# Performance work log

Measured on AMD Instinct MI355X. Metric: run time of the kernel, lower is better.

Reference implementation:

```python
import jax, jax.numpy as jnp
import numpy as np

V, E, H2, T = 50000, 256, 512, 16  # vocab, embed, hidden_dim, tagset
H = H2 // 2                        # per-direction hidden
START, STOP = 14, 15
NEG = -10000.0


def setup_inputs() -> dict:
    key = jax.random.key(0)
    ks = jax.random.split(key, 13)
    s = 0.08
    tokens = jax.random.randint(ks[0], (32, 512), 0, V)
    embed_table = jax.random.normal(ks[1], (V, E), jnp.float32)
    Wi_f = jax.random.normal(ks[2], (4 * H, E), jnp.float32) * s
    Wh_f = jax.random.normal(ks[3], (4 * H, H), jnp.float32) * s
    bi_f = jnp.zeros((4 * H,), jnp.float32)
    bh_f = jnp.zeros((4 * H,), jnp.float32)
    Wi_b = jax.random.normal(ks[4], (4 * H, E), jnp.float32) * s
    Wh_b = jax.random.normal(ks[5], (4 * H, H), jnp.float32) * s
    bi_b = jnp.zeros((4 * H,), jnp.float32)
    bh_b = jnp.zeros((4 * H,), jnp.float32)
    Wt = jax.random.normal(ks[6], (T, H2), jnp.float32) * s
    bt = jnp.zeros((T,), jnp.float32)
    trans = jax.random.normal(ks[7], (T, T), jnp.float32)
    trans = trans.at[START, :].set(NEG).at[:, STOP].set(NEG)
    return {"tokens": tokens, "embed_table": embed_table,
            "Wi_f": Wi_f, "Wh_f": Wh_f, "bi_f": bi_f, "bh_f": bh_f,
            "Wi_b": Wi_b, "Wh_b": Wh_b, "bi_b": bi_b, "bh_b": bh_b,
            "Wt": Wt, "bt": bt, "transitions": trans}


def _lstm_dir(x, Wi, Wh, bi, bh, reverse=False):
    # x: [S, B, E] -> h seq [S, B, H], PyTorch gate order i,f,g,o
    S, B, _ = x.shape
    xs = x[::-1] if reverse else x
    pre = jnp.einsum('sbe,ge->sbg', xs, Wi) + bi + bh  # precompute input GEMM

    def step(carry, z_t):
        h, c = carry
        z = z_t + h @ Wh.T  # [B, 4H]
        i, f, g, o = jnp.split(z, 4, axis=-1)
        c = jax.nn.sigmoid(f) * c + jax.nn.sigmoid(i) * jnp.tanh(g)
        h = jax.nn.sigmoid(o) * jnp.tanh(c)
        return (h, c), h

    h0 = jnp.zeros((B, H), x.dtype)
    _, hs = jax.lax.scan(step, (h0, h0), pre)
    return hs[::-1] if reverse else hs


def reference(tokens, embed_table, Wi_f, Wh_f, bi_f, bh_f,
              Wi_b, Wh_b, bi_b, bh_b, Wt, bt, transitions):
    x = embed_table[tokens]                # [B, S, E]
    x = jnp.transpose(x, (1, 0, 2))        # [S, B, E] seq-first like nn.LSTM
    hf = _lstm_dir(x, Wi_f, Wh_f, bi_f, bh_f, reverse=False)
    hb = _lstm_dir(x, Wi_b, Wh_b, bi_b, bh_b, reverse=True)
    feats = jnp.concatenate([hf, hb], axis=-1)           # [S, B, 2H]
    emissions = jnp.einsum('sbh,th->sbt', feats, Wt) + bt  # [S, B, T]

    B = tokens.shape[0]
    alpha0 = jnp.full((B, T), NEG, jnp.float32).at[:, START].set(0.0)

    def crf_step(alpha, emit_t):
        # alpha: [B, T_prev]; transitions[next, prev]; emit_t: [B, T_next]
        scores = alpha[:, None, :] + transitions[None, :, :] + emit_t[:, :, None]
        return jax.nn.logsumexp(scores, axis=2), None

    alpha, _ = jax.lax.scan(crf_step, alpha0, emissions)
    log_Z = jax.nn.logsumexp(alpha + transitions[STOP][None, :], axis=1)  # [B]
    return log_Z
```

## Files before the change

### kernel.cpp

```cpp
#include <hip/hip_runtime.h>
#include <hip/hip_bf16.h>
#include <stdint.h>

typedef __attribute__((ext_vector_type(4))) float f32x4;
typedef __attribute__((ext_vector_type(8))) short bf16x8;

#define SENT 0xFFFFFFFFFFFFFFFFULL

#define WS_XBF   0u
#define WS_WIR   8388608u
#define WS_BIAS  9437184u
#define WS_PRE   9445376u
#define WS_HALL  76554240u
#define WS_CTL   93364224u
#define WS_EMIS  93368320u
#define WS_CHK   94416896u
#define WS_FLG   WS_CHK

__device__ __forceinline__ unsigned short f2bf(float x) {
    union { float f; unsigned int u; } v; v.f = x;
    return (unsigned short)((v.u + 0x7FFFu + ((v.u >> 16) & 1u)) >> 16);
}
__device__ __forceinline__ float bf2f(unsigned short b) {
    union { float f; unsigned int u; } v; v.u = ((unsigned int)b) << 16; return v.f;
}
__device__ __forceinline__ unsigned int pack2(float a, float b) {
    return (unsigned int)f2bf(a) | ((unsigned int)f2bf(b) << 16);
}
__device__ __forceinline__ float sigf(float x)  { return 1.0f / (1.0f + __expf(-x)); }
__device__ __forceinline__ float tanhf_(float x){ return 1.0f - 2.0f / (__expf(2.0f * x) + 1.0f); }

__global__ __launch_bounds__(256) void k_prep(
    const int* __restrict__ tokens, const float* __restrict__ embed,
    const float* __restrict__ Wi_f, const float* __restrict__ Wi_b,
    const float* __restrict__ bi_f, const float* __restrict__ bh_f,
    const float* __restrict__ bi_b, const float* __restrict__ bh_b,
    char* __restrict__ ws)
{
    int blk = blockIdx.x, tid = threadIdx.x;
    unsigned short* xbf  = (unsigned short*)(ws + WS_XBF);
    unsigned short* wir  = (unsigned short*)(ws + WS_WIR);
    float* biasr         = (float*)(ws + WS_BIAS);
    if (blk < 2048) {
        int rr = tid >> 5, cc = tid & 31;
        int r = blk * 8 + rr;
        int s = r >> 5, b = r & 31;
        int tok = tokens[b * 512 + s];
        int k = cc * 8;
        const float* src = embed + (size_t)tok * 256 + k;
        float4 a = *(const float4*)src;
        float4 c = *(const float4*)(src + 4);
        uint4 o; o.x = pack2(a.x, a.y); o.y = pack2(a.z, a.w);
        o.z = pack2(c.x, c.y); o.w = pack2(c.z, c.w);
        *(uint4*)(xbf + (size_t)r * 256 + k) = o;
    } else if (blk < 2304) {
        int rr = tid >> 5, cc = tid & 31;
        int rowp = (blk - 2048) * 8 + rr;
        int dir = rowp >> 10, q = rowp & 1023;
        int j = q >> 8, rs = q & 255;
        int g = rs >> 6, hl = rs & 63;
        int srow = g * 256 + j * 64 + hl;
        const float* W = dir ? Wi_b : Wi_f;
        int k = cc * 8;
        const float* src = W + (size_t)srow * 256 + k;
        float4 a = *(const float4*)src;
        float4 c = *(const float4*)(src + 4);
        uint4 o; o.x = pack2(a.x, a.y); o.y = pack2(a.z, a.w);
        o.z = pack2(c.x, c.y); o.w = pack2(c.z, c.w);
        *(uint4*)(wir + (size_t)rowp * 256 + k) = o;
        if (cc == 0)
            biasr[rowp] = dir ? (bi_b[srow] + bh_b[srow]) : (bi_f[srow] + bh_f[srow]);
    } else {
        if (blk == 2304 && tid < 16)
            ((unsigned int*)(ws + WS_CTL))[tid] = 0u;
        if (blk == 2305) {
            unsigned int* flg = (unsigned int*)(ws + WS_FLG);
            for (int u = tid; u < 2 * 513 * 4 * 16; u += 256) flg[u] = 0u;
        }
        size_t g = (size_t)(blk - 2304) * 256 + tid;
        uint4* hall4 = (uint4*)(ws + WS_HALL);
        const unsigned int NF = 0xFFFFFFFFu;
        for (size_t u = g; u < 1050624u; u += 65536u) {
            size_t slot = (u >> 10) % 513u;
            uint4 val;
            if (slot == 0) { val.x = 0u; val.y = 0u; val.z = 0u; val.w = 0u; }
            else           { val.x = NF; val.y = NF; val.z = NF; val.w = NF; }
            hall4[u] = val;
        }
    }
}

__global__ __launch_bounds__(256) void k_pregemm(char* __restrict__ ws)
{
    __shared__ unsigned short Asb[128 * 136];
    __shared__ unsigned short Bsb[64 * 136];
    const unsigned short* xbf = (const unsigned short*)(ws + WS_XBF);
    const unsigned short* wir = (const unsigned short*)(ws + WS_WIR);
    const float* biasr        = (const float*)(ws + WS_BIAS);
    unsigned short* pre       = (unsigned short*)(ws + WS_PRE);
    int blk = blockIdx.x, tid = threadIdx.x;
    int mb = blk >> 5, nb = blk & 31;
    int Mbase = mb * 128, Nbase = nb * 64;
    int w = tid >> 6, l = tid & 63, col = l & 15, quad = l >> 4;
    f32x4 acc[4][2];
    #pragma unroll
    for (int a = 0; a < 4; ++a)
        #pragma unroll
        for (int b = 0; b < 2; ++b) acc[a][b] = (f32x4){0.f, 0.f, 0.f, 0.f};

    for (int kh = 0; kh < 2; ++kh) {
        __syncthreads();
        #pragma unroll
        for (int i = 0; i < 8; ++i) {
            int c = tid + i * 256;
            int row = c >> 4, c16 = c & 15;
            uint4 v = *(const uint4*)(xbf + ((size_t)(Mbase + row) * 256 + kh * 128 + c16 * 8));
            *(uint4*)(Asb + row * 136 + c16 * 8) = v;
        }
        #pragma unroll
        for (int i = 0; i < 4; ++i) {
            int c = tid + i * 256;
            int row = c >> 4, c16 = c & 15;
            uint4 v = *(const uint4*)(wir + ((size_t)(Nbase + row) * 256 + kh * 128 + c16 * 8));
            *(uint4*)(Bsb + row * 136 + c16 * 8) = v;
        }
        __syncthreads();
        int mhalf = w >> 1, nh = w & 1;
        #pragma unroll
        for (int kt = 0; kt < 4; ++kt) {
            bf16x8 bfr[2];
            #pragma unroll
            for (int nn = 0; nn < 2; ++nn)
                bfr[nn] = *(const bf16x8*)(Bsb + (16 * (nh * 2 + nn) + col) * 136 + kt * 32 + quad * 8);
            #pragma unroll
            for (int mm = 0; mm < 4; ++mm) {
                bf16x8 afr = *(const bf16x8*)(Asb + (16 * (mhalf * 4 + mm) + col) * 136 + kt * 32 + quad * 8);
                #pragma unroll
                for (int nn = 0; nn < 2; ++nn)
                    acc[mm][nn] = __builtin_amdgcn_mfma_f32_16x16x32_bf16(afr, bfr[nn], acc[mm][nn], 0, 0, 0);
            }
        }
    }
    #pragma unroll
    for (int mm = 0; mm < 4; ++mm) {
        int m_t = (w >> 1) * 4 + mm;
        int s = (Mbase >> 5) + (m_t >> 1);
        int bhalf = m_t & 1;
        #pragma unroll
        for (int nn = 0; nn < 2; ++nn) {
            int ncol = Nbase + 16 * ((w & 1) * 2 + nn) + col;
            int dir = ncol >> 10, j = (ncol >> 8) & 3, r = ncol & 255;
            int g = r >> 6, hl16 = (r >> 4) & 3;
            int tidp = (bhalf * 4 + hl16) * 64 + l;
            float bv = biasr[ncol];
            f32x4 a = acc[mm][nn];
            uint2 o;
            o.x = pack2(a[0] + bv, a[1] + bv);
            o.y = pack2(a[2] + bv, a[3] + bv);
            size_t off = (((size_t)(dir * 512 + s) * 4 + j) * 512 + tidp) * 16 + g * 4;
            *(uint2*)(pre + off) = o;
        }
    }
}

__global__ __launch_bounds__(512, 2) void k_rec(
    const float* __restrict__ Wh_f, const float* __restrict__ Wh_b, char* __restrict__ ws)
{
    __shared__ unsigned short hbuf[32 * 264];
    __shared__ unsigned short hst[8 * 16 * 20];
    __shared__ int sRole;
    int tid = threadIdx.x;

    if (tid == 0) {
        int xcd;
        asm volatile("s_getreg_b32 %0, hwreg(HW_REG_XCC_ID)" : "=s"(xcd));
        xcd &= 7;
        unsigned int* ctl = (unsigned int*)(ws + WS_CTL);
        unsigned int slot = __hip_atomic_fetch_add(&ctl[xcd], 1u,
                              __ATOMIC_RELAXED, __HIP_MEMORY_SCOPE_AGENT);
        int role = -1;
        if (slot < 8u) {
            if (slot == 7u) {
                unsigned int expv = 0u;
                __hip_atomic_compare_exchange_strong(&ctl[8], &expv, (unsigned int)(xcd + 1),
                    __ATOMIC_RELAXED, __ATOMIC_RELAXED, __HIP_MEMORY_SCOPE_AGENT);
            }
            unsigned int ts; long gc = 0;
            do {
                ts = __hip_atomic_fetch_add(&ctl[8], 0u,
                        __ATOMIC_RELAXED, __HIP_MEMORY_SCOPE_AGENT);
            } while (ts == 0u && ++gc < (1L << 26));
            if (ts == (unsigned int)(xcd + 1)) role = (int)slot;
        }
        sRole = role;
    }
    __syncthreads();
    int role = sRole;
    if (role < 0) return;
    int dir = role >> 2, j = role & 3;

    int w = tid >> 6, l = tid & 63, col = l & 15, quad = l >> 4;
    int m = w >> 2, hl16 = w & 3;
    const float* Wh = dir ? Wh_b : Wh_f;
    const unsigned short* pre = (const unsigned short*)(ws + WS_PRE);
    unsigned short* hall      = (unsigned short*)(ws + WS_HALL);
    unsigned int* flags       = (unsigned int*)(ws + WS_FLG);

    bf16x8 wf[4][8];
    #pragma unroll
    for (int g = 0; g < 4; ++g) {
        int grow = g * 256 + j * 64 + hl16 * 16 + col;
        #pragma unroll
        for (int kt = 0; kt < 8; ++kt) {
            const float* src = Wh + (size_t)grow * 256 + kt * 32 + quad * 8;
            float4 x0 = *(const float4*)src;
            float4 x1 = *(const float4*)(src + 4);
            bf16x8 f;
            f[0] = (short)f2bf(x0.x); f[1] = (short)f2bf(x0.y);
            f[2] = (short)f2bf(x0.z); f[3] = (short)f2bf(x0.w);
            f[4] = (short)f2bf(x1.x); f[5] = (short)f2bf(x1.y);
            f[6] = (short)f2bf(x1.z); f[7] = (short)f2bf(x1.w);
            wf[g][kt] = f;
        }
    }
    for (int u = tid; u < 1280; u += 512) ((unsigned int*)hst)[u] = 0;
    __syncthreads();

    float cst[4] = {0.f, 0.f, 0.f, 0.f};
    size_t hbase_u = (size_t)dir * 513 * 8192;
    int row0 = tid >> 6, c8 = tid & 63;
    bool ownl = (c8 >= j * 16) && (c8 < j * 16 + 16);
    int pollj = (l < 4 && l != j) ? l : -1;

    for (int st = 0; st < 512; ++st) {
        int s = dir ? (511 - st) : st;
        const uint4* pp = (const uint4*)(pre + ((((size_t)(dir * 512 + s)) * 4 + j) * 512 + tid) * 16);
        uint4 p0 = pp[0], p1 = pp[1];

        unsigned short* hsl = hall + hbase_u + (size_t)st * 8192;

        if (st > 0) {
            unsigned int* fl = flags + ((size_t)(dir * 513 + st)) * 64;
            int got = (pollj < 0) ? 1 : 0;
            int rnd = 0;
            while (!__all(got)) {
                if (!got) {
                    unsigned int expv = 0u;
                    __hip_atomic_compare_exchange_strong(fl + pollj * 16, &expv, 0u,
                        __ATOMIC_RELAXED, __ATOMIC_RELAXED, __HIP_MEMORY_SCOPE_WORKGROUP);
                    got = (expv != 0u) ? 1 : 0;
                }
                if (++rnd > (1 << 20)) break;
            }
            asm volatile("" ::: "memory");
        }

        unsigned long long v[4];
        if (ownl) {
            int lc = c8 * 4 - j * 64;
            int hl = lc >> 4, c4 = lc & 15;
            #pragma unroll
            for (int i = 0; i < 4; ++i) {
                int row = row0 + i * 8;
                int wp = (row >> 4) * 4 + hl, r_in = row & 15;
                v[i] = *(const unsigned long long*)(hst + wp * 320 + r_in * 20 + c4);
            }
        } else {
            #pragma unroll
            for (int i = 0; i < 4; ++i)
                v[i] = *(const unsigned long long*)(hsl + (size_t)(tid + i * 512) * 4);
        }
        #pragma unroll
        for (int i = 0; i < 4; ++i)
            *(unsigned long long*)(hbuf + (row0 + i * 8) * 264 + c8 * 4) = v[i];
        __syncthreads();

        f32x4 acc[4];
        #pragma unroll
        for (int g = 0; g < 4; ++g) acc[g] = (f32x4){0.f, 0.f, 0.f, 0.f};
        #pragma unroll
        for (int kt = 0; kt < 8; ++kt) {
            bf16x8 af = *(const bf16x8*)(hbuf + (m * 16 + col) * 264 + kt * 32 + quad * 8);
            #pragma unroll
            for (int g = 0; g < 4; ++g)
                acc[g] = __builtin_amdgcn_mfma_f32_16x16x32_bf16(af, wf[g][kt], acc[g], 0, 0, 0);
        }
        unsigned int pw[8] = {p0.x, p0.y, p0.z, p0.w, p1.x, p1.y, p1.z, p1.w};
        float z[4][4];
        #pragma unroll
        for (int g = 0; g < 4; ++g) {
            #pragma unroll
            for (int r2 = 0; r2 < 2; ++r2) {
                unsigned int u = pw[g * 2 + r2];
                z[g][r2 * 2]     = acc[g][r2 * 2]     + bf2f((unsigned short)(u & 0xffff));
                z[g][r2 * 2 + 1] = acc[g][r2 * 2 + 1] + bf2f((unsigned short)(u >> 16));
            }
        }
        unsigned short hb16[4];
        #pragma unroll
        for (int r = 0; r < 4; ++r) {
            float ci = sigf(z[1][r]) * cst[r] + sigf(z[0][r]) * tanhf_(z[2][r]);
            cst[r] = ci;
            hb16[r] = f2bf(sigf(z[3][r]) * tanhf_(ci));
        }
        unsigned short* hw = hst + w * 320;
        #pragma unroll
        for (int r = 0; r < 4; ++r) hw[(quad * 4 + r) * 20 + col] = hb16[r];
        int rrow = l >> 2, cpart = l & 3;
        unsigned long long hv = *(const unsigned long long*)(hw + rrow * 20 + cpart * 4);
        size_t dsto = hbase_u + (size_t)(st + 1) * 8192 + (size_t)(m * 16 + rrow) * 256
                    + j * 64 + hl16 * 16 + cpart * 4;
        *(unsigned long long*)(hall + dsto) = hv;
        __syncthreads();
        if (tid == 0)
            (void)__hip_atomic_exchange(flags + ((size_t)(dir * 513 + st + 1)) * 64 + j * 16, 1u,
                                        __ATOMIC_RELAXED, __HIP_MEMORY_SCOPE_WORKGROUP);
    }
}

__global__ __launch_bounds__(256) void k_emis(
    const float* __restrict__ Wt, const float* __restrict__ bt, char* __restrict__ ws)
{
    __shared__ float WtL[16 * 528];
    __shared__ unsigned short hrow[16 * 536];
    __shared__ float btL[16];
    int blk = blockIdx.x, tid = threadIdx.x;
    int sbb = blk * 16;
    int s = sbb >> 5, bbase = sbb & 31;
    const unsigned short* hall = (const unsigned short*)(ws + WS_HALL);
    float* emis = (float*)(ws + WS_EMIS);
    #pragma unroll
    for (int i = 0; i < 8; ++i) {
        int c = tid + i * 256;
        int trow = c >> 7, c128 = c & 127;
        float4 v = *(const float4*)(Wt + (size_t)trow * 512 + c128 * 4);
        *(float4*)(WtL + trow * 528 + c128 * 4) = v;
    }
    #pragma unroll
    for (int i = 0; i < 4; ++i) {
        int c = tid + i * 256;
        int row = c >> 6, c6 = c & 63, half = c6 >> 5, c16 = c6 & 31;
        size_t base = half == 0 ? (size_t)(s + 1) * 8192 : ((size_t)513 + (512 - s)) * 8192;
        uint4 v = *(const uint4*)(hall + base + (size_t)(bbase + row) * 256 + c16 * 8);
        *(uint4*)(hrow + row * 536 + half * 256 + c16 * 8) = v;
    }
    if (tid < 16) btL[tid] = bt[tid];
    __syncthreads();
    int t = tid >> 4, i = tid & 15;
    float acc = btL[t];
    const float* wrow = WtL + t * 528;
    const unsigned short* hr = hrow + i * 536;
    #pragma unroll 8
    for (int k = 0; k < 512; k += 4) {
        uint2 hu = *(const uint2*)(hr + k);
        float4 wv = *(const float4*)(wrow + k);
        acc += bf2f((unsigned short)(hu.x & 0xffff)) * wv.x
             + bf2f((unsigned short)(hu.x >> 16))    * wv.y
             + bf2f((unsigned short)(hu.y & 0xffff)) * wv.z
             + bf2f((unsigned short)(hu.y >> 16))    * wv.w;
    }
    emis[((size_t)(bbase + i) * 512 + s) * 16 + t] = acc;
}

__global__ __launch_bounds__(256) void k_crfc(const float* __restrict__ trans, char* __restrict__ ws)
{
    __shared__ float trL[16 * 17];
    __shared__ float est[16 * 16];
    __shared__ float Pb[2][16 * 17];
    int blk = blockIdx.x, tid = threadIdx.x;
    int b = blk >> 5, c = blk & 31;
    int t = tid >> 4, p = tid & 15;
    const float* emis = (const float*)(ws + WS_EMIS);
    float* chk = (float*)(ws + WS_CHK);
    trL[t * 17 + p] = trans[t * 16 + p];
    est[t * 16 + p] = emis[((size_t)b * 512 + c * 16 + t) * 16 + p];
    __syncthreads();
    float tr[16];
    #pragma unroll
    for (int q = 0; q < 16; ++q) tr[q] = trL[t * 17 + q];
    float out = trL[t * 17 + p] + est[0 * 16 + t];
    Pb[0][t * 17 + p] = out;
    __syncthreads();
    int cur = 0;
    for (int si = 1; si < 16; ++si) {
        float v[16]; float mx = -3.0e38f;
        #pragma unroll
        for (int q = 0; q < 16; ++q) { v[q] = tr[q] + Pb[cur][q * 17 + p]; mx = fmaxf(mx, v[q]); }
        float ss = 0.f;
        #pragma unroll
        for (int q = 0; q < 16; ++q) ss += __expf(v[q] - mx);
        out = est[si * 16 + t] + mx + __logf(ss);
        Pb[1 - cur][t * 17 + p] = out;
        __syncthreads();
        cur = 1 - cur;
    }
    chk[(size_t)(b * 32 + c) * 256 + t * 16 + p] = out;
}

__global__ __launch_bounds__(256) void k_crff(
    const float* __restrict__ trans, char* __restrict__ ws, float* __restrict__ out)
{
    __shared__ float Cst[16 * 17];
    __shared__ float Pb[2][16 * 17];
    __shared__ float af[16];
    int b = blockIdx.x, tid = threadIdx.x;
    int t = tid >> 4, p = tid & 15;
    const float* chk = (const float*)(ws + WS_CHK);
    Pb[0][t * 17 + p] = chk[(size_t)(b * 32) * 256 + t * 16 + p];
    __syncthreads();
    int cur = 0;
    for (int ci = 1; ci < 32; ++ci) {
        Cst[t * 17 + p] = chk[(size_t)(b * 32 + ci) * 256 + t * 16 + p];
        __syncthreads();
        float v[16]; float mx = -3.0e38f;
        #pragma unroll
        for (int q = 0; q < 16; ++q) { v[q] = Cst[t * 17 + q] + Pb[cur][q * 17 + p]; mx = fmaxf(mx, v[q]); }
        float ss = 0.f;
        #pragma unroll
        for (int q = 0; q < 16; ++q) ss += __expf(v[q] - mx);
        float outv = mx + __logf(ss);
        Pb[1 - cur][t * 17 + p] = outv;
        __syncthreads();
        cur = 1 - cur;
    }
    float vfin = Pb[cur][t * 17 + p] + ((p == 14) ? 0.0f : -10000.0f);
    Cst[t * 17 + p] = vfin;
    __syncthreads();
    if (tid < 16) {
        float mx = -3.0e38f;
        for (int q = 0; q < 16; ++q) mx = fmaxf(mx, Cst[tid * 17 + q]);
        float ss = 0.f;
        for (int q = 0; q < 16; ++q) ss += __expf(Cst[tid * 17 + q] - mx);
        af[tid] = mx + __logf(ss) + trans[15 * 16 + tid];
    }
    __syncthreads();
    if (tid == 0) {
        float mx = -3.0e38f;
        for (int q = 0; q < 16; ++q) mx = fmaxf(mx, af[q]);
        float ss = 0.f;
        for (int q = 0; q < 16; ++q) ss += __expf(af[q] - mx);
        out[b] = mx + __logf(ss);
    }
}

extern "C" void kernel_launch(void* const* d_in, const int* in_sizes, int n_in,
                              void* d_out, int out_size, void* d_ws, size_t ws_size,
                              hipStream_t stream)
{
    const int*   tokens = (const int*)d_in[0];
    const float* embed  = (const float*)d_in[1];
    const float* Wi_f   = (const float*)d_in[2];
    const float* Wh_f   = (const float*)d_in[3];
    const float* bi_f   = (const float*)d_in[4];
    const float* bh_f   = (const float*)d_in[5];
    const float* Wi_b   = (const float*)d_in[6];
    const float* Wh_b   = (const float*)d_in[7];
    const float* bi_b   = (const float*)d_in[8];
    const float* bh_b   = (const float*)d_in[9];
    const float* Wt     = (const float*)d_in[10];
    const float* bt     = (const float*)d_in[11];
    const float* trans  = (const float*)d_in[12];
    char* ws = (char*)d_ws;
    float* out = (float*)d_out;

    hipLaunchKernelGGL(k_prep, dim3(2560), dim3(256), 0, stream,
                       tokens, embed, Wi_f, Wi_b, bi_f, bh_f, bi_b, bh_b, ws);
    hipLaunchKernelGGL(k_pregemm, dim3(4096), dim3(256), 0, stream, ws);
    hipLaunchKernelGGL(k_rec, dim3(128), dim3(512), 0, stream, Wh_f, Wh_b, ws);
    hipLaunchKernelGGL(k_emis, dim3(1024), dim3(256), 0, stream, Wt, bt, ws);
    hipLaunchKernelGGL(k_crfc, dim3(1024), dim3(256), 0, stream, trans, ws);
    hipLaunchKernelGGL(k_crff, dim3(32), dim3(256), 0, stream, trans, ws, out);
}
```

Baseline: 1.814 ms.

## Read recurrent hidden state directly from global memory, pad LDS to force one block per CU

The recurrent LSTM kernel stops staging h through the LDS hbuf/hst buffers and loads the MFMA A-fragments straight from the global hidden-state history. Each lane now writes its bf16 h values with scalar stores, and the pre-step syncthreads and own-slice LDS path are removed. A large static and dynamic LDS padding is added so only one workgroup fits per CU, presumably to spread the cross-block spinning recurrence across more CUs. The spin-wait bound is lowered and the sentinel init is set to zero. The risks are scattered 2-byte global stores, and global reads that may see another block's rows before they are visible, since only relaxed flags guard them.

After: 2.198 ms. 1.21x slower.

```diff
diff --git a/kernel.cpp b/kernel.cpp
--- a/kernel.cpp
+++ b/kernel.cpp
@@ -4,8 +4,6 @@
 
 typedef __attribute__((ext_vector_type(4))) float f32x4;
 typedef __attribute__((ext_vector_type(8))) short bf16x8;
-
-#define SENT 0xFFFFFFFFFFFFFFFFULL
 
 #define WS_XBF   0u
 #define WS_WIR   8388608u
@@ -79,12 +77,11 @@
         }
         size_t g = (size_t)(blk - 2304) * 256 + tid;
         uint4* hall4 = (uint4*)(ws + WS_HALL);
-        const unsigned int NF = 0xFFFFFFFFu;
         for (size_t u = g; u < 1050624u; u += 65536u) {
             size_t slot = (u >> 10) % 513u;
             uint4 val;
             if (slot == 0) { val.x = 0u; val.y = 0u; val.z = 0u; val.w = 0u; }
-            else           { val.x = NF; val.y = NF; val.z = NF; val.w = NF; }
+            else           { val.x = 0u; val.y = 0u; val.z = 0u; val.w = 0u; }
             hall4[u] = val;
         }
     }
@@ -166,12 +163,14 @@
 __global__ __launch_bounds__(512, 2) void k_rec(
     const float* __restrict__ Wh_f, const float* __restrict__ Wh_b, char* __restrict__ ws)
 {
-    __shared__ unsigned short hbuf[32 * 264];
-    __shared__ unsigned short hst[8 * 16 * 20];
+    extern __shared__ char dynpad[];
+    __shared__ char stpad[61440];
     __shared__ int sRole;
     int tid = threadIdx.x;
 
     if (tid == 0) {
+        ((volatile char*)stpad)[0] = 0;
+        ((volatile char*)dynpad)[0] = 0;
         int xcd;
         asm volatile("s_getreg_b32 %0, hwreg(HW_REG_XCC_ID)" : "=s"(xcd));
         xcd &= 7;
@@ -223,21 +222,15 @@
             wf[g][kt] = f;
         }
     }
-    for (int u = tid; u < 1280; u += 512) ((unsigned int*)hst)[u] = 0;
-    __syncthreads();
 
     float cst[4] = {0.f, 0.f, 0.f, 0.f};
     size_t hbase_u = (size_t)dir * 513 * 8192;
-    int row0 = tid >> 6, c8 = tid & 63;
-    bool ownl = (c8 >= j * 16) && (c8 < j * 16 + 16);
     int pollj = (l < 4 && l != j) ? l : -1;
 
     for (int st = 0; st < 512; ++st) {
         int s = dir ? (511 - st) : st;
         const uint4* pp = (const uint4*)(pre + ((((size_t)(dir * 512 + s)) * 4 + j) * 512 + tid) * 16);
         uint4 p0 = pp[0], p1 = pp[1];
-
-        unsigned short* hsl = hall + hbase_u + (size_t)st * 8192;
 
         if (st > 0) {
             unsigned int* fl = flags + ((size_t)(dir * 513 + st)) * 64;
@@ -250,40 +243,26 @@
                         __ATOMIC_RELAXED, __ATOMIC_RELAXED, __HIP_MEMORY_SCOPE_WORKGROUP);
                     got = (expv != 0u) ? 1 : 0;
                 }
-                if (++rnd > (1 << 20)) break;
+                if (++rnd > (1 << 17)) break;
             }
             asm volatile("" ::: "memory");
         }
 
-        unsigned long long v[4];
-        if (ownl) {
-            int lc = c8 * 4 - j * 64;
-            int hl = lc >> 4, c4 = lc & 15;
-            #pragma unroll
-            for (int i = 0; i < 4; ++i) {
-                int row = row0 + i * 8;
-                int wp = (row >> 4) * 4 + hl, r_in = row & 15;
-                v[i] = *(const unsigned long long*)(hst + wp * 320 + r_in * 20 + c4);
-            }
-        } else {
-            #pragma unroll
-            for (int i = 0; i < 4; ++i)
-                v[i] = *(const unsigned long long*)(hsl + (size_t)(tid + i * 512) * 4);
-        }
-        #pragma unroll
-        for (int i = 0; i < 4; ++i)
-            *(unsigned long long*)(hbuf + (row0 + i * 8) * 264 + c8 * 4) = v[i];
-        __syncthreads();
+        const unsigned short* hrp = hall + hbase_u + (size_t)st * 8192
+                                  + (size_t)(m * 16 + col) * 256 + quad * 8;
+        bf16x8 af[8];
+        #pragma unroll
+        for (int kt = 0; kt < 8; ++kt)
+            af[kt] = *(const bf16x8*)(hrp + kt * 32);
 
         f32x4 acc[4];
         #pragma unroll
         for (int g = 0; g < 4; ++g) acc[g] = (f32x4){0.f, 0.f, 0.f, 0.f};
         #pragma unroll
         for (int kt = 0; kt < 8; ++kt) {
-            bf16x8 af = *(const bf16x8*)(hbuf + (m * 16 + col) * 264 + kt * 32 + quad * 8);
             #pragma unroll
             for (int g = 0; g < 4; ++g)
-                acc[g] = __builtin_amdgcn_mfma_f32_16x16x32_bf16(af, wf[g][kt], acc[g], 0, 0, 0);
+                acc[g] = __builtin_amdgcn_mfma_f32_16x16x32_bf16(af[kt], wf[g][kt], acc[g], 0, 0, 0);
         }
         unsigned int pw[8] = {p0.x, p0.y, p0.z, p0.w, p1.x, p1.y, p1.z, p1.w};
         float z[4][4];
@@ -303,14 +282,11 @@
             cst[r] = ci;
             hb16[r] = f2bf(sigf(z[3][r]) * tanhf_(ci));
         }
-        unsigned short* hw = hst + w * 320;
-        #pragma unroll
-        for (int r = 0; r < 4; ++r) hw[(quad * 4 + r) * 20 + col] = hb16[r];
-        int rrow = l >> 2, cpart = l & 3;
-        unsigned long long hv = *(const unsigned long long*)(hw + rrow * 20 + cpart * 4);
-        size_t dsto = hbase_u + (size_t)(st + 1) * 8192 + (size_t)(m * 16 + rrow) * 256
-                    + j * 64 + hl16 * 16 + cpart * 4;
-        *(unsigned long long*)(hall + dsto) = hv;
+        size_t dstb = hbase_u + (size_t)(st + 1) * 8192
+                    + (size_t)(m * 16 + quad * 4) * 256 + j * 64 + hl16 * 16 + col;
+        #pragma unroll
+        for (int r = 0; r < 4; ++r)
+            *(hall + dstb + (size_t)r * 256) = hb16[r];
         __syncthreads();
         if (tid == 0)
             (void)__hip_atomic_exchange(flags + ((size_t)(dir * 513 + st + 1)) * 64 + j * 16, 1u,
@@ -466,7 +442,7 @@
     hipLaunchKernelGGL(k_prep, dim3(2560), dim3(256), 0, stream,
                        tokens, embed, Wi_f, Wi_b, bi_f, bh_f, bi_b, bh_b, ws);
     hipLaunchKernelGGL(k_pregemm, dim3(4096), dim3(256), 0, stream, ws);
-    hipLaunchKernelGGL(k_rec, dim3(128), dim3(512), 0, stream, Wh_f, Wh_b, ws);
+    hipLaunchKernelGGL(k_rec, dim3(128), dim3(512), 49152, stream, Wh_f, Wh_b, ws);
     hipLaunchKernelGGL(k_emis, dim3(1024), dim3(256), 0, stream, Wt, bt, ws);
     hipLaunchKernelGGL(k_crfc, dim3(1024), dim3(256), 0, stream, trans, ws);
     hipLaunchKernelGGL(k_crff, dim3(32), dim3(256), 0, stream, trans, ws, out);
```
